# Kernel optimization log

Measured on AMD Instinct MI355X. Metric: run time of the kernel, lower is better.

The kernel has to match this reference:

```python
import jax, jax.numpy as jnp
import numpy as np

NEG_BIG = -1.0e9


def setup_inputs() -> dict:
    key = jax.random.key(0)
    kq, kk, kv, km = jax.random.split(key, 4)
    B, Lq, Lk, D = 16, 2048, 2048, 128
    queries = jax.random.normal(kq, (B, Lq, D), dtype=jnp.float32)
    keys = jax.random.normal(kk, (B, Lk, D), dtype=jnp.float32)
    values = jax.random.normal(kv, (B, Lk, D), dtype=jnp.float32)
    mask = (jax.random.uniform(km, (Lk,)) > 0.8).astype(jnp.float32)
    return {"queries": queries, "keys": keys, "values": values, "mask": mask}


def reference(queries, keys, values, mask):
    d = keys.shape[-1]
    # scores: [B, Lq, Lk]
    scores = jnp.einsum("bqd,bkd->bqk", queries, keys) / jnp.sqrt(jnp.float32(d))
    masked = scores + mask[None, None, :] * NEG_BIG
    attn = jax.nn.softmax(masked, axis=-1)
    # dropout is identity in eval / p=0.0
    return jnp.einsum("bqk,bkd->bqd", attn, values)
```

## Files before the change

### kernel.cpp

```cpp
#include <hip/hip_runtime.h>
#include <hip/hip_bf16.h>


#define B_    16
#define LQ_   2048
#define LK_   2048
#define DIM_  128
#define NTH   256
#define SCALE_ 0.08838834764831845f
#define LOG2E_ 1.4426950408889634f
#define SC2_   (SCALE_ * LOG2E_)
#define NEGBIG -1.0e9f
#define PS 72

typedef __attribute__((ext_vector_type(8))) short bf16x8;
typedef __attribute__((ext_vector_type(4))) float f32x4;

#define GLDS(gsrc, ldst) \
  __builtin_amdgcn_global_load_lds( \
      (const __attribute__((address_space(1))) unsigned int*)(gsrc), \
      (__attribute__((address_space(3))) unsigned int*)(ldst), 16, 0, 0)

#define MFMA16(A, Bv, C) __builtin_amdgcn_mfma_f32_16x16x32_bf16((A), (Bv), (C), 0, 0, 0)

static __device__ __forceinline__ unsigned short f2bf(float f) {
    unsigned int u = __builtin_bit_cast(unsigned int, f);
    u += 0x7fff + ((u >> 16) & 1);
    return (unsigned short)(u >> 16);
}

__global__ __launch_bounds__(256) void build_idx(const float* __restrict__ Mk,
                                                 int* __restrict__ hdr,
                                                 int* __restrict__ idx)
{
    __shared__ int sc[256];
    int t = threadIdx.x;
    int keep[8], loc[8];
    int c = 0;
    #pragma unroll
    for (int j = 0; j < 8; ++j) {
        keep[j] = (Mk[t * 8 + j] < 0.5f) ? 1 : 0;
        loc[j] = c;
        c += keep[j];
    }
    sc[t] = c;
    __syncthreads();
    for (int off = 1; off < 256; off <<= 1) {
        int v = (t >= off) ? sc[t - off] : 0;
        __syncthreads();
        sc[t] += v;
        __syncthreads();
    }
    int base = sc[t] - c;
    #pragma unroll
    for (int j = 0; j < 8; ++j)
        if (keep[j]) idx[base + loc[j]] = t * 8 + j;
    if (t == 255) hdr[0] = sc[255];
}

__global__ __launch_bounds__(NTH) void pack_kv(
    const float* __restrict__ K, const float* __restrict__ V,
    const int* __restrict__ hdr, const int* __restrict__ idx,
    unsigned short* __restrict__ Kb, unsigned short* __restrict__ Vtb)
{
    const int cnt = hdr[0];
    int bid = blockIdx.x;
    if (bid < 2048) {
        int gid = bid * NTH + threadIdx.x;
        int c  = gid & 15;
        int r2 = (gid >> 4) & 63;
        int T  = gid >> 10;
        int slot = (r2 & 32) + 2 * (r2 & 15) + ((r2 >> 4) & 1);
        int j = (T & 31) * 64 + slot;
        int key = (j < cnt) ? idx[j] : 0;
        const float4* s4 = (const float4*)(K + ((size_t)(T >> 5) * LK_ + key) * DIM_ + c * 8);
        float4 a = s4[0], bq = s4[1];
        bf16x8 h = { (short)f2bf(a.x),  (short)f2bf(a.y),  (short)f2bf(a.z),  (short)f2bf(a.w),
                     (short)f2bf(bq.x), (short)f2bf(bq.y), (short)f2bf(bq.z), (short)f2bf(bq.w) };
        *(bf16x8*)(Kb + (size_t)T * 8192 + r2 * 128 + ((c ^ (r2 & 15)) * 8)) = h;
    } else {
        int T = bid - 2048;
        int w4 = threadIdx.x >> 6, lane = threadIdx.x & 63;
        const float* vb = V + (size_t)(T >> 5) * LK_ * DIM_;
        const int* ix = idx + (T & 31) * 64;
        int jbase = (T & 31) * 64;
        unsigned short* db = Vtb + (size_t)T * 8192;
        #pragma unroll
        for (int half = 0; half < 2; ++half) {
            int d = half * 64 + lane;
            #pragma unroll
            for (int cb = 0; cb < 8; cb += 4) {
                int c = cb + w4;
                float v[8];
                #pragma unroll
                for (int kk = 0; kk < 8; ++kk) {
                    int j = c * 8 + kk;
                    int key = (jbase + j < cnt) ? ix[j] : 0;
                    v[kk] = vb[(size_t)key * DIM_ + d];
                }
                bf16x8 h = { (short)f2bf(v[0]), (short)f2bf(v[1]), (short)f2bf(v[2]), (short)f2bf(v[3]),
                             (short)f2bf(v[4]), (short)f2bf(v[5]), (short)f2bf(v[6]), (short)f2bf(v[7]) };
                *(bf16x8*)(db + (c >> 2) * 4096 + d * 32 + (c & 3) * 8) = h;
            }
        }
    }
}

__global__ __launch_bounds__(NTH, 2) void attn_mfma6(
    const float* __restrict__ Q, const unsigned short* __restrict__ Kb,
    const unsigned short* __restrict__ Vtb, const int* __restrict__ hdr,
    float* __restrict__ O)
{
    __shared__ __align__(16) unsigned short sKa[8192];
    __shared__ __align__(16) unsigned short sKb_[8192];
    __shared__ __align__(16) unsigned short sP[64 * PS];
    __shared__ float sLp[64];

    const int tid  = threadIdx.x;
    const int w    = tid >> 6, lane = tid & 63;
    const int quad = lane >> 4, l15 = lane & 15;
    const int rg   = (w & 1) * 32;
    const int wh   = w >> 1;
    const int kh   = wh * 32;

    const int bid = blockIdx.x;
    const int grp = bid >> 3;
    const int b   = (bid & 7) + 8 * (grp & 1);
    const int q0  = (grp >> 1) * 64;

    const int cnt = hdr[0];
    const int n = (((cnt + 63) >> 6) + 1) & ~1;

    bf16x8 vone;
    #pragma unroll
    for (int j = 0; j < 8; ++j) vone[j] = (short)0x3F80;

    const int voff = wh * 4096 + l15 * 32 + quad * 8;
    const unsigned short* vtb = Vtb + (size_t)(b * 32) * 8192 + voff;

    const char* kbase = (const char*)Kb + (size_t)(b * 32) * 16384;

    #pragma unroll
    for (int j = 0; j < 4; ++j) {
        int o = (j * 4 + w) * 1024;
        GLDS(kbase + o + lane * 16, (char*)sKa + o);
    }

    bf16x8 aQ[2][4];
    {
        const float4* Qg = (const float4*)(Q + ((size_t)b * LQ_ + q0) * DIM_);
        #pragma unroll
        for (int h = 0; h < 2; ++h) {
            #pragma unroll
            for (int it = 0; it < 4; ++it) {
                int i2 = tid + it * NTH;
                int r = i2 >> 5, c4 = i2 & 31;
                float4 v = Qg[(h * 32 + r) * 32 + c4];
                ushort4 hh = { f2bf(v.x * SC2_), f2bf(v.y * SC2_),
                               f2bf(v.z * SC2_), f2bf(v.w * SC2_) };
                *(ushort4*)&sP[r * 128 + (((c4 >> 1) ^ (r & 15)) * 8) + (c4 & 1) * 4] = hh;
            }
            __syncthreads();
            if ((rg >> 5) == h) {
                #pragma unroll
                for (int rs = 0; rs < 2; ++rs)
                    #pragma unroll
                    for (int ks = 0; ks < 4; ++ks)
                        aQ[rs][ks] = *(const bf16x8*)&sP[(rs * 16 + l15) * 128 +
                                                         (((ks * 4 + quad) ^ l15) * 8)];
            }
            __syncthreads();
        }
    }

    f32x4 acc[2][8], lacc[2];
    #pragma unroll
    for (int rs = 0; rs < 2; ++rs) {
        lacc[rs] = (f32x4){0.f, 0.f, 0.f, 0.f};
        #pragma unroll
        for (int dt = 0; dt < 8; ++dt) acc[rs][dt] = (f32x4){0.f, 0.f, 0.f, 0.f};
    }

    f32x4 s_[2][2];
    bf16x8 bvA[8], bvB[8];

#define QK_TILE(RD) do {                                                       \
    f32x4 c00 = (f32x4){0.f,0.f,0.f,0.f};                                      \
    f32x4 c01 = (f32x4){0.f,0.f,0.f,0.f};                                      \
    f32x4 c10 = (f32x4){0.f,0.f,0.f,0.f};                                      \
    f32x4 c11 = (f32x4){0.f,0.f,0.f,0.f};                                      \
    _Pragma("unroll")                                                          \
    for (int ks = 0; ks < 4; ++ks) {                                           \
        int co = ((ks * 4 + quad) ^ l15) * 8;                                  \
        bf16x8 bk0 = *(const bf16x8*)&(RD)[(kh + l15) * 128 + co];             \
        bf16x8 bk1 = *(const bf16x8*)&(RD)[(kh + 16 + l15) * 128 + co];        \
        c00 = MFMA16(aQ[0][ks], bk0, c00);                                     \
        c10 = MFMA16(aQ[1][ks], bk0, c10);                                     \
        c01 = MFMA16(aQ[0][ks], bk1, c01);                                     \
        c11 = MFMA16(aQ[1][ks], bk1, c11);                                     \
    }                                                                          \
    s_[0][0] = c00; s_[0][1] = c01; s_[1][0] = c10; s_[1][1] = c11;            \
} while (0)

#define SOFTMAX_AP(TI) do {                                                    \
    int slot0 = (TI) * 64 + kh + 2 * l15;                                      \
    unsigned umask = (slot0     < cnt ? 0x0000FFFFu : 0u) |                    \
                     (slot0 + 1 < cnt ? 0xFFFF0000u : 0u);                     \
    _Pragma("unroll")                                                          \
    for (int rs = 0; rs < 2; ++rs)                                             \
        _Pragma("unroll")                                                      \
        for (int r = 0; r < 4; ++r) {                                          \
            float p0 = __builtin_amdgcn_exp2f(s_[rs][0][r]);                   \
            float p1 = __builtin_amdgcn_exp2f(s_[rs][1][r]);                   \
            int row = rg + rs * 16 + quad * 4 + r;                             \
            unsigned pk = __builtin_amdgcn_perm(                               \
                __builtin_bit_cast(unsigned, p1),                              \
                __builtin_bit_cast(unsigned, p0), 0x07060302u) & umask;        \
            *(unsigned*)&sP[row * PS + kh + 2 * l15] = pk;                     \
        }                                                                      \
    aP0 = *(const bf16x8*)&sP[(rg + l15) * PS + kh + quad * 8];                \
    aP1 = *(const bf16x8*)&sP[(rg + 16 + l15) * PS + kh + quad * 8];           \
} while (0)

#define BODY(RD, WR, I, BVC, BVN) do {                                         \
    __syncthreads();                 \
    {                                                                          \
        const unsigned short* vsrc = vtb + (size_t)((I) + 1) * 8192;           \
        _Pragma("unroll")                                                      \
        for (int dt = 0; dt < 8; ++dt) BVN[dt] = *(const bf16x8*)(vsrc + dt * 512); \
    }                                                                          \
    {                                                                          \
        int t2 = (I) + 2; if (t2 > n - 1) t2 = n - 1;                          \
        const char* ksrc = kbase + (size_t)t2 * 16384;                         \
        _Pragma("unroll")                                                      \
        for (int j = 0; j < 4; ++j) {                                          \
            int o = (j * 4 + w) * 1024;                                        \
            GLDS(ksrc + o + lane * 16, (char*)(WR) + o);                       \
        }                                                                      \
    }                                                                          \
    bf16x8 aP0, aP1;                                                           \
    SOFTMAX_AP(I);                                                             \
    __builtin_amdgcn_s_setprio(1);                                             \
    QK_TILE(RD);                                      \
    lacc[0] = MFMA16(aP0, vone, lacc[0]);                                      \
    lacc[1] = MFMA16(aP1, vone, lacc[1]);                                      \
    _Pragma("unroll")                                                          \
    for (int dt = 0; dt < 8; ++dt) {                                           \
        acc[0][dt] = MFMA16(aP0, BVC[dt], acc[0][dt]);                         \
        acc[1][dt] = MFMA16(aP1, BVC[dt], acc[1][dt]);                         \
    }                                                                          \
    __builtin_amdgcn_s_setprio(0);                                             \
} while (0)

    {
        #pragma unroll
        for (int dt = 0; dt < 8; ++dt) bvA[dt] = *(const bf16x8*)(vtb + dt * 512);
        const char* ksrc = kbase + 16384;
        #pragma unroll
        for (int j = 0; j < 4; ++j) {
            int o = (j * 4 + w) * 1024;
            GLDS(ksrc + o + lane * 16, (char*)sKb_ + o);
        }
    }
    QK_TILE(sKa);

    int i = 0;
    for (; i + 1 < n - 1; i += 2) {
        BODY(sKb_, sKa, i,     bvA, bvB);
        BODY(sKa, sKb_, i + 1, bvB, bvA);
    }
    if (i < n - 1) BODY(sKb_, sKa, i, bvA, bvB);

    {
        bf16x8 aP0, aP1;
        SOFTMAX_AP(n - 1);
        lacc[0] = MFMA16(aP0, vone, lacc[0]);
        lacc[1] = MFMA16(aP1, vone, lacc[1]);
        #pragma unroll
        for (int dt = 0; dt < 8; ++dt) {
            acc[0][dt] = MFMA16(aP0, bvB[dt], acc[0][dt]);
            acc[1][dt] = MFMA16(aP1, bvB[dt], acc[1][dt]);
        }
    }
#undef BODY
#undef SOFTMAX_AP
#undef QK_TILE

    __syncthreads();

    float* sOw = (rg == 0) ? (float*)sKa : (float*)sKb_;
    if (wh == 1) {
        #pragma unroll
        for (int rs = 0; rs < 2; ++rs)
            #pragma unroll
            for (int r = 0; r < 4; ++r) {
                int lrow = rs * 16 + quad * 4 + r;
                #pragma unroll
                for (int dt = 0; dt < 8; ++dt)
                    sOw[lrow * 128 + dt * 16 + l15] = acc[rs][dt][r];
                if (l15 == 0) sLp[rg + lrow] = lacc[rs][r];
            }
    }
    __syncthreads();
    if (wh == 0) {
        float* Og = O + ((size_t)b * LQ_ + q0 + rg) * DIM_;
        #pragma unroll
        for (int rs = 0; rs < 2; ++rs)
            #pragma unroll
            for (int r = 0; r < 4; ++r) {
                int lrow = rs * 16 + quad * 4 + r;
                float inv = 1.0f / (lacc[rs][r] + sLp[rg + lrow]);
                #pragma unroll
                for (int dt = 0; dt < 8; ++dt)
                    Og[(size_t)lrow * DIM_ + dt * 16 + l15] =
                        (acc[rs][dt][r] + sOw[lrow * 128 + dt * 16 + l15]) * inv;
            }
    }
}

#define QS 136
#define VS 72
__global__ __launch_bounds__(NTH, 2) void attn_fallback(
    const float* __restrict__ Q, const float* __restrict__ K,
    const float* __restrict__ V, const float* __restrict__ Mk,
    float* __restrict__ O)
{
    __shared__ __align__(16) unsigned short sQ[64][QS];
    __shared__ __align__(16) unsigned short sK[64][QS];
    __shared__ __align__(16) unsigned short sVt[DIM_][VS];
    __shared__ __align__(16) unsigned short sPf[64][VS];
    __shared__ float sB[64];

    const int tid  = threadIdx.x;
    const int w    = tid >> 6, lane = tid & 63;
    const int quad = lane >> 4, l15 = lane & 15;
    const int bid = blockIdx.x;
    const int grp = bid >> 3;
    const int b   = (bid & 7) + 8 * (grp & 1);
    const int q0  = (grp >> 1) * 64;

    {
        const float4* Qg = (const float4*)(Q + ((size_t)b * LQ_ + q0) * DIM_);
        #pragma unroll
        for (int it = 0; it < 8; ++it) {
            int i = tid + it * NTH;
            int r = i >> 5, c4 = i & 31;
            float4 v = Qg[r * 32 + c4];
            ushort4 h = { f2bf(v.x), f2bf(v.y), f2bf(v.z), f2bf(v.w) };
            *(ushort4*)&sQ[r][c4 * 4] = h;
        }
    }
    __syncthreads();
    bf16x8 aQ[4];
    #pragma unroll
    for (int ks = 0; ks < 4; ++ks)
        aQ[ks] = *(const bf16x8*)&sQ[w * 16 + l15][ks * 32 + quad * 8];

    float m_i[4], l_i[4];
    f32x4 acc[8];
    #pragma unroll
    for (int r = 0; r < 4; ++r) { m_i[r] = -3.0e38f; l_i[r] = 0.f; }
    #pragma unroll
    for (int dt = 0; dt < 8; ++dt) acc[dt] = (f32x4){0.f, 0.f, 0.f, 0.f};

    for (int k0 = 0; k0 < LK_; k0 += 64) {
        const float4* Kg = (const float4*)(K + ((size_t)b * LK_ + k0) * DIM_);
        const float4* Vg = (const float4*)(V + ((size_t)b * LK_ + k0) * DIM_);
        #pragma unroll
        for (int it = 0; it < 8; ++it) {
            int i = tid + it * NTH;
            int r = i >> 5, c4 = i & 31;
            float4 kv = Kg[r * 32 + c4];
            ushort4 h = { f2bf(kv.x), f2bf(kv.y), f2bf(kv.z), f2bf(kv.w) };
            *(ushort4*)&sK[r][c4 * 4] = h;
            float4 vv = Vg[r * 32 + c4];
            int d = c4 * 4;
            sVt[d + 0][r] = f2bf(vv.x);
            sVt[d + 1][r] = f2bf(vv.y);
            sVt[d + 2][r] = f2bf(vv.z);
            sVt[d + 3][r] = f2bf(vv.w);
        }
        if (tid < 64) sB[tid] = Mk[k0 + tid] * NEGBIG;
        __syncthreads();

        f32x4 s[4];
        #pragma unroll
        for (int kt = 0; kt < 4; ++kt) {
            f32x4 c = (f32x4){0.f, 0.f, 0.f, 0.f};
            #pragma unroll
            for (int ks = 0; ks < 4; ++ks) {
                bf16x8 bk = *(const bf16x8*)&sK[kt * 16 + l15][ks * 32 + quad * 8];
                c = __builtin_amdgcn_mfma_f32_16x16x32_bf16(aQ[ks], bk, c, 0, 0, 0);
            }
            float bias = sB[kt * 16 + l15];
            #pragma unroll
            for (int r = 0; r < 4; ++r) s[kt][r] = c[r] * SCALE_ + bias;
        }
        #pragma unroll
        for (int r = 0; r < 4; ++r) {
            float mx = fmaxf(fmaxf(s[0][r], s[1][r]), fmaxf(s[2][r], s[3][r]));
            #pragma unroll
            for (int off = 1; off < 16; off <<= 1) mx = fmaxf(mx, __shfl_xor(mx, off));
            float mn = fmaxf(m_i[r], mx);
            float al = __expf(m_i[r] - mn);
            m_i[r] = mn;
            float rsum = 0.f;
            #pragma unroll
            for (int kt = 0; kt < 4; ++kt) {
                float p = __expf(s[kt][r] - mn);
                rsum += p;
                sPf[w * 16 + quad * 4 + r][kt * 16 + l15] = f2bf(p);
            }
            #pragma unroll
            for (int off = 1; off < 16; off <<= 1) rsum += __shfl_xor(rsum, off);
            l_i[r] = l_i[r] * al + rsum;
            #pragma unroll
            for (int dt = 0; dt < 8; ++dt) acc[dt][r] *= al;
        }
        bf16x8 aP0 = *(const bf16x8*)&sPf[w * 16 + l15][quad * 8];
        bf16x8 aP1 = *(const bf16x8*)&sPf[w * 16 + l15][32 + quad * 8];
        #pragma unroll
        for (int dt = 0; dt < 8; ++dt) {
            bf16x8 bv0 = *(const bf16x8*)&sVt[dt * 16 + l15][quad * 8];
            bf16x8 bv1 = *(const bf16x8*)&sVt[dt * 16 + l15][32 + quad * 8];
            acc[dt] = __builtin_amdgcn_mfma_f32_16x16x32_bf16(aP0, bv0, acc[dt], 0, 0, 0);
            acc[dt] = __builtin_amdgcn_mfma_f32_16x16x32_bf16(aP1, bv1, acc[dt], 0, 0, 0);
        }
        __syncthreads();
    }
    float* Og = O + ((size_t)b * LQ_ + q0 + w * 16) * DIM_;
    #pragma unroll
    for (int r = 0; r < 4; ++r) {
        float inv = 1.0f / l_i[r];
        int row = quad * 4 + r;
        #pragma unroll
        for (int dt = 0; dt < 8; ++dt)
            Og[(size_t)row * DIM_ + dt * 16 + l15] = acc[dt][r] * inv;
    }
}

extern "C" void kernel_launch(void* const* d_in, const int* in_sizes, int n_in,
                              void* d_out, int out_size, void* d_ws, size_t ws_size,
                              hipStream_t stream)
{
    const float* Q  = (const float*)d_in[0];
    const float* K  = (const float*)d_in[1];
    const float* V  = (const float*)d_in[2];
    const float* Mk = (const float*)d_in[3];
    float* O = (float*)d_out;

    const size_t seg  = (size_t)B_ * LK_ * DIM_ * 2;
    const size_t need = 16384 + 2 * seg;
    if (ws_size >= need) {
        int* hdr = (int*)d_ws;
        int* idx = hdr + 16;
        unsigned short* Kb  = (unsigned short*)((char*)d_ws + 16384);
        unsigned short* Vtb = Kb + seg / 2;
        hipLaunchKernelGGL(build_idx, dim3(1),    dim3(256), 0, stream, Mk, hdr, idx);
        hipLaunchKernelGGL(pack_kv,   dim3(2560), dim3(NTH), 0, stream, K, V, hdr, idx, Kb, Vtb);
        hipLaunchKernelGGL(attn_mfma6, dim3(512), dim3(NTH), 0, stream, Q, Kb, Vtb, hdr, O);
    } else {
        hipLaunchKernelGGL(attn_fallback, dim3(512), dim3(NTH), 0, stream, Q, K, V, Mk, O);
    }
}
```

Baseline: 146.9 us.

## Split attention block across eight waves with 16-row tiles and direct V loads

The attention kernel now runs 512 threads (eight waves) per block, and each wave owns 16 query rows instead of 32. This halves the per-wave accumulator and Q-fragment registers, and launch bounds ask for four blocks per CU to raise occupancy. The register double-buffered V prefetch is dropped: V fragments for the current tile are loaded inside each iteration, which may expose global-load latency. K tiles are loaded with fewer LDS copies per wave, while the per-tile MFMA count per wave halves and the QK B-operand LDS reads are duplicated across more waves.

```diff
diff --git a/kernel.cpp b/kernel.cpp
--- a/kernel.cpp
+++ b/kernel.cpp
@@ -7,6 +7,7 @@
 #define LK_   2048
 #define DIM_  128
 #define NTH   256
+#define ATH   512
 #define SCALE_ 0.08838834764831845f
 #define LOG2E_ 1.4426950408889634f
 #define SC2_   (SCALE_ * LOG2E_)
@@ -106,7 +107,7 @@
     }
 }
 
-__global__ __launch_bounds__(NTH, 2) void attn_mfma6(
+__global__ __launch_bounds__(ATH, 4) void attn_mfma8(
     const float* __restrict__ Q, const unsigned short* __restrict__ Kb,
     const unsigned short* __restrict__ Vtb, const int* __restrict__ hdr,
     float* __restrict__ O)
@@ -119,8 +120,8 @@
     const int tid  = threadIdx.x;
     const int w    = tid >> 6, lane = tid & 63;
     const int quad = lane >> 4, l15 = lane & 15;
-    const int rg   = (w & 1) * 32;
-    const int wh   = w >> 1;
+    const int rg   = (w & 3) * 16;
+    const int wh   = w >> 2;
     const int kh   = wh * 32;
 
     const int bid = blockIdx.x;
@@ -141,19 +142,19 @@
     const char* kbase = (const char*)Kb + (size_t)(b * 32) * 16384;
 
     #pragma unroll
-    for (int j = 0; j < 4; ++j) {
-        int o = (j * 4 + w) * 1024;
+    for (int j = 0; j < 2; ++j) {
+        int o = (j * 8 + w) * 1024;
         GLDS(kbase + o + lane * 16, (char*)sKa + o);
     }
 
-    bf16x8 aQ[2][4];
+    bf16x8 aQ[4];
     {
         const float4* Qg = (const float4*)(Q + ((size_t)b * LQ_ + q0) * DIM_);
         #pragma unroll
         for (int h = 0; h < 2; ++h) {
             #pragma unroll
-            for (int it = 0; it < 4; ++it) {
-                int i2 = tid + it * NTH;
+            for (int it = 0; it < 2; ++it) {
+                int i2 = tid + it * ATH;
                 int r = i2 >> 5, c4 = i2 & 31;
                 float4 v = Qg[(h * 32 + r) * 32 + c4];
                 ushort4 hh = { f2bf(v.x * SC2_), f2bf(v.y * SC2_),
@@ -163,43 +164,33 @@
             __syncthreads();
             if ((rg >> 5) == h) {
                 #pragma unroll
-                for (int rs = 0; rs < 2; ++rs)
-                    #pragma unroll
-                    for (int ks = 0; ks < 4; ++ks)
-                        aQ[rs][ks] = *(const bf16x8*)&sP[(rs * 16 + l15) * 128 +
-                                                         (((ks * 4 + quad) ^ l15) * 8)];
+                for (int ks = 0; ks < 4; ++ks)
+                    aQ[ks] = *(const bf16x8*)&sP[((rg & 16) + l15) * 128 +
+                                                 (((ks * 4 + quad) ^ l15) * 8)];
             }
             __syncthreads();
         }
     }
 
-    f32x4 acc[2][8], lacc[2];
-    #pragma unroll
-    for (int rs = 0; rs < 2; ++rs) {
-        lacc[rs] = (f32x4){0.f, 0.f, 0.f, 0.f};
-        #pragma unroll
-        for (int dt = 0; dt < 8; ++dt) acc[rs][dt] = (f32x4){0.f, 0.f, 0.f, 0.f};
-    }
-
-    f32x4 s_[2][2];
-    bf16x8 bvA[8], bvB[8];
+    f32x4 acc[8], lacc;
+    lacc = (f32x4){0.f, 0.f, 0.f, 0.f};
+    #pragma unroll
+    for (int dt = 0; dt < 8; ++dt) acc[dt] = (f32x4){0.f, 0.f, 0.f, 0.f};
+
+    f32x4 s_[2];
 
 #define QK_TILE(RD) do {                                                       \
-    f32x4 c00 = (f32x4){0.f,0.f,0.f,0.f};                                      \
-    f32x4 c01 = (f32x4){0.f,0.f,0.f,0.f};                                      \
-    f32x4 c10 = (f32x4){0.f,0.f,0.f,0.f};                                      \
-    f32x4 c11 = (f32x4){0.f,0.f,0.f,0.f};                                      \
+    f32x4 c0 = (f32x4){0.f,0.f,0.f,0.f};                                       \
+    f32x4 c1 = (f32x4){0.f,0.f,0.f,0.f};                                       \
     _Pragma("unroll")                                                          \
     for (int ks = 0; ks < 4; ++ks) {                                           \
         int co = ((ks * 4 + quad) ^ l15) * 8;                                  \
         bf16x8 bk0 = *(const bf16x8*)&(RD)[(kh + l15) * 128 + co];             \
         bf16x8 bk1 = *(const bf16x8*)&(RD)[(kh + 16 + l15) * 128 + co];        \
-        c00 = MFMA16(aQ[0][ks], bk0, c00);                                     \
-        c10 = MFMA16(aQ[1][ks], bk0, c10);                                     \
-        c01 = MFMA16(aQ[0][ks], bk1, c01);                                     \
-        c11 = MFMA16(aQ[1][ks], bk1, c11);                                     \
+        c0 = MFMA16(aQ[ks], bk0, c0);                                          \
+        c1 = MFMA16(aQ[ks], bk1, c1);                                          \
     }                                                                          \
-    s_[0][0] = c00; s_[0][1] = c01; s_[1][0] = c10; s_[1][1] = c11;            \
+    s_[0] = c0; s_[1] = c1;                                                    \
 } while (0)
 
 #define SOFTMAX_AP(TI) do {                                                    \
@@ -207,58 +198,49 @@
     unsigned umask = (slot0     < cnt ? 0x0000FFFFu : 0u) |                    \
                      (slot0 + 1 < cnt ? 0xFFFF0000u : 0u);                     \
     _Pragma("unroll")                                                          \
-    for (int rs = 0; rs < 2; ++rs)                                             \
-        _Pragma("unroll")                                                      \
-        for (int r = 0; r < 4; ++r) {                                          \
-            float p0 = __builtin_amdgcn_exp2f(s_[rs][0][r]);                   \
-            float p1 = __builtin_amdgcn_exp2f(s_[rs][1][r]);                   \
-            int row = rg + rs * 16 + quad * 4 + r;                             \
-            unsigned pk = __builtin_amdgcn_perm(                               \
-                __builtin_bit_cast(unsigned, p1),                              \
-                __builtin_bit_cast(unsigned, p0), 0x07060302u) & umask;        \
-            *(unsigned*)&sP[row * PS + kh + 2 * l15] = pk;                     \
-        }                                                                      \
-    aP0 = *(const bf16x8*)&sP[(rg + l15) * PS + kh + quad * 8];                \
-    aP1 = *(const bf16x8*)&sP[(rg + 16 + l15) * PS + kh + quad * 8];           \
+    for (int r = 0; r < 4; ++r) {                                              \
+        float p0 = __builtin_amdgcn_exp2f(s_[0][r]);                           \
+        float p1 = __builtin_amdgcn_exp2f(s_[1][r]);                           \
+        int row = rg + quad * 4 + r;                                           \
+        unsigned pk = __builtin_amdgcn_perm(                                   \
+            __builtin_bit_cast(unsigned, p1),                                  \
+            __builtin_bit_cast(unsigned, p0), 0x07060302u) & umask;            \
+        *(unsigned*)&sP[row * PS + kh + 2 * l15] = pk;                         \
+    }                                                                          \
+    aP = *(const bf16x8*)&sP[(rg + l15) * PS + kh + quad * 8];                 \
 } while (0)
 
-#define BODY(RD, WR, I, BVC, BVN) do {                                         \
-    __syncthreads();                 \
-    {                                                                          \
-        const unsigned short* vsrc = vtb + (size_t)((I) + 1) * 8192;           \
-        _Pragma("unroll")                                                      \
-        for (int dt = 0; dt < 8; ++dt) BVN[dt] = *(const bf16x8*)(vsrc + dt * 512); \
-    }                                                                          \
+#define BODY(RD, WR, I) do {                                                   \
+    __syncthreads();            \
+    const unsigned short* vsrc = vtb + (size_t)(I) * 8192;                     \
+    bf16x8 bv[8];                                                              \
+    _Pragma("unroll")                                                          \
+    for (int dt = 0; dt < 8; ++dt) bv[dt] = *(const bf16x8*)(vsrc + dt * 512); \
     {                                                                          \
         int t2 = (I) + 2; if (t2 > n - 1) t2 = n - 1;                          \
         const char* ksrc = kbase + (size_t)t2 * 16384;                         \
         _Pragma("unroll")                                                      \
-        for (int j = 0; j < 4; ++j) {                                          \
-            int o = (j * 4 + w) * 1024;                                        \
+        for (int j = 0; j < 2; ++j) {                                          \
+            int o = (j * 8 + w) * 1024;                                        \
             GLDS(ksrc + o + lane * 16, (char*)(WR) + o);                       \
         }                                                                      \
     }                                                                          \
-    bf16x8 aP0, aP1;                                                           \
+    bf16x8 aP;                                                                 \
     SOFTMAX_AP(I);                                                             \
     __builtin_amdgcn_s_setprio(1);                                             \
     QK_TILE(RD);                                      \
-    lacc[0] = MFMA16(aP0, vone, lacc[0]);                                      \
-    lacc[1] = MFMA16(aP1, vone, lacc[1]);                                      \
+    lacc = MFMA16(aP, vone, lacc);                                             \
     _Pragma("unroll")                                                          \
-    for (int dt = 0; dt < 8; ++dt) {                                           \
-        acc[0][dt] = MFMA16(aP0, BVC[dt], acc[0][dt]);                         \
-        acc[1][dt] = MFMA16(aP1, BVC[dt], acc[1][dt]);                         \
-    }                                                                          \
+    for (int dt = 0; dt < 8; ++dt)                                             \
+        acc[dt] = MFMA16(aP, bv[dt], acc[dt]);                                 \
     __builtin_amdgcn_s_setprio(0);                                             \
 } while (0)
 
     {
-        #pragma unroll
-        for (int dt = 0; dt < 8; ++dt) bvA[dt] = *(const bf16x8*)(vtb + dt * 512);
         const char* ksrc = kbase + 16384;
         #pragma unroll
-        for (int j = 0; j < 4; ++j) {
-            int o = (j * 4 + w) * 1024;
+        for (int j = 0; j < 2; ++j) {
+            int o = (j * 8 + w) * 1024;
             GLDS(ksrc + o + lane * 16, (char*)sKb_ + o);
         }
     }
@@ -266,21 +248,22 @@
 
     int i = 0;
     for (; i + 1 < n - 1; i += 2) {
-        BODY(sKb_, sKa, i,     bvA, bvB);
-        BODY(sKa, sKb_, i + 1, bvB, bvA);
-    }
-    if (i < n - 1) BODY(sKb_, sKa, i, bvA, bvB);
+        BODY(sKb_, sKa, i);
+        BODY(sKa, sKb_, i + 1);
+    }
+    if (i < n - 1) BODY(sKb_, sKa, i);
 
     {
-        bf16x8 aP0, aP1;
+        const unsigned short* vsrc = vtb + (size_t)(n - 1) * 8192;
+        bf16x8 bv[8];
+        #pragma unroll
+        for (int dt = 0; dt < 8; ++dt) bv[dt] = *(const bf16x8*)(vsrc + dt * 512);
+        bf16x8 aP;
         SOFTMAX_AP(n - 1);
-        lacc[0] = MFMA16(aP0, vone, lacc[0]);
-        lacc[1] = MFMA16(aP1, vone, lacc[1]);
-        #pragma unroll
-        for (int dt = 0; dt < 8; ++dt) {
-            acc[0][dt] = MFMA16(aP0, bvB[dt], acc[0][dt]);
-            acc[1][dt] = MFMA16(aP1, bvB[dt], acc[1][dt]);
-        }
+        lacc = MFMA16(aP, vone, lacc);
+        #pragma unroll
+        for (int dt = 0; dt < 8; ++dt)
+            acc[dt] = MFMA16(aP, bv[dt], acc[dt]);
     }
 #undef BODY
 #undef SOFTMAX_AP
@@ -288,33 +271,30 @@
 
     __syncthreads();
 
-    float* sOw = (rg == 0) ? (float*)sKa : (float*)sKb_;
+    float* sOw = (rg < 32) ? ((float*)sKa + (rg & 16) * 128)
+                           : ((float*)sKb_ + (rg & 16) * 128);
     if (wh == 1) {
         #pragma unroll
-        for (int rs = 0; rs < 2; ++rs)
-            #pragma unroll
-            for (int r = 0; r < 4; ++r) {
-                int lrow = rs * 16 + quad * 4 + r;
-                #pragma unroll
-                for (int dt = 0; dt < 8; ++dt)
-                    sOw[lrow * 128 + dt * 16 + l15] = acc[rs][dt][r];
-                if (l15 == 0) sLp[rg + lrow] = lacc[rs][r];
-            }
+        for (int r = 0; r < 4; ++r) {
+            int lrow = quad * 4 + r;
+            #pragma unroll
+            for (int dt = 0; dt < 8; ++dt)
+                sOw[lrow * 128 + dt * 16 + l15] = acc[dt][r];
+            if (l15 == 0) sLp[rg + lrow] = lacc[r];
+        }
     }
     __syncthreads();
     if (wh == 0) {
         float* Og = O + ((size_t)b * LQ_ + q0 + rg) * DIM_;
         #pragma unroll
-        for (int rs = 0; rs < 2; ++rs)
-            #pragma unroll
-            for (int r = 0; r < 4; ++r) {
-                int lrow = rs * 16 + quad * 4 + r;
-                float inv = 1.0f / (lacc[rs][r] + sLp[rg + lrow]);
-                #pragma unroll
-                for (int dt = 0; dt < 8; ++dt)
-                    Og[(size_t)lrow * DIM_ + dt * 16 + l15] =
-                        (acc[rs][dt][r] + sOw[lrow * 128 + dt * 16 + l15]) * inv;
-            }
+        for (int r = 0; r < 4; ++r) {
+            int lrow = quad * 4 + r;
+            float inv = 1.0f / (lacc[r] + sLp[rg + lrow]);
+            #pragma unroll
+            for (int dt = 0; dt < 8; ++dt)
+                Og[(size_t)lrow * DIM_ + dt * 16 + l15] =
+                    (acc[dt][r] + sOw[lrow * 128 + dt * 16 + l15]) * inv;
+        }
     }
 }
 
@@ -458,7 +438,7 @@
         unsigned short* Vtb = Kb + seg / 2;
         hipLaunchKernelGGL(build_idx, dim3(1),    dim3(256), 0, stream, Mk, hdr, idx);
         hipLaunchKernelGGL(pack_kv,   dim3(2560), dim3(NTH), 0, stream, K, V, hdr, idx, Kb, Vtb);
-        hipLaunchKernelGGL(attn_mfma6, dim3(512), dim3(NTH), 0, stream, Q, Kb, Vtb, hdr, O);
+        hipLaunchKernelGGL(attn_mfma8, dim3(512), dim3(ATH), 0, stream, Q, Kb, Vtb, hdr, O);
     } else {
         hipLaunchKernelGGL(attn_fallback, dim3(512), dim3(NTH), 0, stream, Q, K, V, Mk, O);
     }
```

Result: slower. 174.6 us (+18.9%).

## Load K tiles directly into registers in MFMA fragment layout, drop LDS staging

Applied to the files above, without the earlier changes.

The pack kernel now writes K in a per-lane MFMA-fragment order, so the attention kernel can load each lane's K operands straight from global memory into registers instead of staging them through LDS with global_load_lds. The K prefetch is double-buffered in registers (bkA/bkB), V loads move to the current iteration, and the software pipeline is restructured so QK runs before softmax each iteration, with the odd-tile epilogue simplified. This removes LDS traffic and the related bank-conflict and sync pressure for K, at the cost of more VGPRs and of exposing global load latency inside each iteration.

```diff
diff --git a/kernel.cpp b/kernel.cpp
--- a/kernel.cpp
+++ b/kernel.cpp
@@ -16,11 +16,6 @@
 typedef __attribute__((ext_vector_type(8))) short bf16x8;
 typedef __attribute__((ext_vector_type(4))) float f32x4;
 
-#define GLDS(gsrc, ldst) \
-  __builtin_amdgcn_global_load_lds( \
-      (const __attribute__((address_space(1))) unsigned int*)(gsrc), \
-      (__attribute__((address_space(3))) unsigned int*)(ldst), 16, 0, 0)
-
 #define MFMA16(A, Bv, C) __builtin_amdgcn_mfma_f32_16x16x32_bf16((A), (Bv), (C), 0, 0, 0)
 
 static __device__ __forceinline__ unsigned short f2bf(float f) {
@@ -68,16 +63,19 @@
     if (bid < 2048) {
         int gid = bid * NTH + threadIdx.x;
         int c  = gid & 15;
-        int r2 = (gid >> 4) & 63;
+        int s  = (gid >> 4) & 63;
         int T  = gid >> 10;
-        int slot = (r2 & 32) + 2 * (r2 & 15) + ((r2 >> 4) & 1);
-        int j = (T & 31) * 64 + slot;
+        int j = (T & 31) * 64 + s;
         int key = (j < cnt) ? idx[j] : 0;
         const float4* s4 = (const float4*)(K + ((size_t)(T >> 5) * LK_ + key) * DIM_ + c * 8);
         float4 a = s4[0], bq = s4[1];
         bf16x8 h = { (short)f2bf(a.x),  (short)f2bf(a.y),  (short)f2bf(a.z),  (short)f2bf(a.w),
                      (short)f2bf(bq.x), (short)f2bf(bq.y), (short)f2bf(bq.z), (short)f2bf(bq.w) };
-        *(bf16x8*)(Kb + (size_t)T * 8192 + r2 * 128 + ((c ^ (r2 & 15)) * 8)) = h;
+        int kc = s >> 5, kt2 = s & 1, l15v = (s >> 1) & 15;
+        int ks = c >> 2, quad = c & 3;
+        int lane = quad * 16 + l15v;
+        *(bf16x8*)(Kb + (size_t)T * 8192 +
+                   (size_t)(((kc * 2 + kt2) * 4 + ks) * 512 + lane * 8)) = h;
     } else {
         int T = bid - 2048;
         int w4 = threadIdx.x >> 6, lane = threadIdx.x & 63;
@@ -106,7 +104,7 @@
     }
 }
 
-__global__ __launch_bounds__(NTH, 2) void attn_mfma6(
+__global__ __launch_bounds__(NTH, 2) void attn_mfma10(
     const float* __restrict__ Q, const unsigned short* __restrict__ Kb,
     const unsigned short* __restrict__ Vtb, const int* __restrict__ hdr,
     float* __restrict__ O)
@@ -129,7 +127,7 @@
     const int q0  = (grp >> 1) * 64;
 
     const int cnt = hdr[0];
-    const int n = (((cnt + 63) >> 6) + 1) & ~1;
+    const int nt = (cnt + 63) >> 6;
 
     bf16x8 vone;
     #pragma unroll
@@ -137,14 +135,8 @@
 
     const int voff = wh * 4096 + l15 * 32 + quad * 8;
     const unsigned short* vtb = Vtb + (size_t)(b * 32) * 8192 + voff;
-
-    const char* kbase = (const char*)Kb + (size_t)(b * 32) * 16384;
-
-    #pragma unroll
-    for (int j = 0; j < 4; ++j) {
-        int o = (j * 4 + w) * 1024;
-        GLDS(kbase + o + lane * 16, (char*)sKa + o);
-    }
+    const int koff = wh * 4096 + lane * 8;
+    const unsigned short* ktb = Kb + (size_t)(b * 32) * 8192 + koff;
 
     bf16x8 aQ[2][4];
     {
@@ -181,23 +173,25 @@
         for (int dt = 0; dt < 8; ++dt) acc[rs][dt] = (f32x4){0.f, 0.f, 0.f, 0.f};
     }
 
-    f32x4 s_[2][2];
-    bf16x8 bvA[8], bvB[8];
-
-#define QK_TILE(RD) do {                                                       \
+    bf16x8 bkA[8], bkB[8];
+
+#define LOADK(BK, TI) do {                                                     \
+    const unsigned short* ksrc = ktb + (size_t)(TI) * 8192;                    \
+    _Pragma("unroll")                                                          \
+    for (int f = 0; f < 8; ++f) BK[f] = *(const bf16x8*)(ksrc + f * 512);      \
+} while (0)
+
+#define QK_TILE(BK) do {                                                       \
     f32x4 c00 = (f32x4){0.f,0.f,0.f,0.f};                                      \
     f32x4 c01 = (f32x4){0.f,0.f,0.f,0.f};                                      \
     f32x4 c10 = (f32x4){0.f,0.f,0.f,0.f};                                      \
     f32x4 c11 = (f32x4){0.f,0.f,0.f,0.f};                                      \
     _Pragma("unroll")                                                          \
     for (int ks = 0; ks < 4; ++ks) {                                           \
-        int co = ((ks * 4 + quad) ^ l15) * 8;                                  \
-        bf16x8 bk0 = *(const bf16x8*)&(RD)[(kh + l15) * 128 + co];             \
-        bf16x8 bk1 = *(const bf16x8*)&(RD)[(kh + 16 + l15) * 128 + co];        \
-        c00 = MFMA16(aQ[0][ks], bk0, c00);                                     \
-        c10 = MFMA16(aQ[1][ks], bk0, c10);                                     \
-        c01 = MFMA16(aQ[0][ks], bk1, c01);                                     \
-        c11 = MFMA16(aQ[1][ks], bk1, c11);                                     \
+        c00 = MFMA16(aQ[0][ks], BK[ks], c00);                                  \
+        c10 = MFMA16(aQ[1][ks], BK[ks], c10);                                  \
+        c01 = MFMA16(aQ[0][ks], BK[4 + ks], c01);                              \
+        c11 = MFMA16(aQ[1][ks], BK[4 + ks], c11);                              \
     }                                                                          \
     s_[0][0] = c00; s_[0][1] = c01; s_[1][0] = c10; s_[1][1] = c11;            \
 } while (0)
@@ -222,71 +216,40 @@
     aP1 = *(const bf16x8*)&sP[(rg + 16 + l15) * PS + kh + quad * 8];           \
 } while (0)
 
-#define BODY(RD, WR, I, BVC, BVN) do {                                         \
-    __syncthreads();                 \
-    {                                                                          \
-        const unsigned short* vsrc = vtb + (size_t)((I) + 1) * 8192;           \
-        _Pragma("unroll")                                                      \
-        for (int dt = 0; dt < 8; ++dt) BVN[dt] = *(const bf16x8*)(vsrc + dt * 512); \
-    }                                                                          \
-    {                                                                          \
-        int t2 = (I) + 2; if (t2 > n - 1) t2 = n - 1;                          \
-        const char* ksrc = kbase + (size_t)t2 * 16384;                         \
-        _Pragma("unroll")                                                      \
-        for (int j = 0; j < 4; ++j) {                                          \
-            int o = (j * 4 + w) * 1024;                                        \
-            GLDS(ksrc + o + lane * 16, (char*)(WR) + o);                       \
-        }                                                                      \
-    }                                                                          \
+#define BODY(CUR, NXT, I) do {                                                 \
+    const unsigned short* vsrc = vtb + (size_t)(I) * 8192;                     \
+    bf16x8 bv[8];                                                              \
+    _Pragma("unroll")                                                          \
+    for (int dt = 0; dt < 8; ++dt) bv[dt] = *(const bf16x8*)(vsrc + dt * 512); \
+    int t2 = (I) + 1; if (t2 > nt - 1) t2 = nt - 1;                            \
+    LOADK(NXT, t2);                                                            \
+    f32x4 s_[2][2];                                                            \
     bf16x8 aP0, aP1;                                                           \
+    QK_TILE(CUR);                                                              \
     SOFTMAX_AP(I);                                                             \
     __builtin_amdgcn_s_setprio(1);                                             \
-    QK_TILE(RD);                                      \
     lacc[0] = MFMA16(aP0, vone, lacc[0]);                                      \
     lacc[1] = MFMA16(aP1, vone, lacc[1]);                                      \
     _Pragma("unroll")                                                          \
     for (int dt = 0; dt < 8; ++dt) {                                           \
-        acc[0][dt] = MFMA16(aP0, BVC[dt], acc[0][dt]);                         \
-        acc[1][dt] = MFMA16(aP1, BVC[dt], acc[1][dt]);                         \
+        acc[0][dt] = MFMA16(aP0, bv[dt], acc[0][dt]);                          \
+        acc[1][dt] = MFMA16(aP1, bv[dt], acc[1][dt]);                          \
     }                                                                          \
     __builtin_amdgcn_s_setprio(0);                                             \
+    __syncthreads();                                                           \
 } while (0)
 
-    {
-        #pragma unroll
-        for (int dt = 0; dt < 8; ++dt) bvA[dt] = *(const bf16x8*)(vtb + dt * 512);
-        const char* ksrc = kbase + 16384;
-        #pragma unroll
-        for (int j = 0; j < 4; ++j) {
-            int o = (j * 4 + w) * 1024;
-            GLDS(ksrc + o + lane * 16, (char*)sKb_ + o);
-        }
-    }
-    QK_TILE(sKa);
-
+    LOADK(bkA, 0);
     int i = 0;
-    for (; i + 1 < n - 1; i += 2) {
-        BODY(sKb_, sKa, i,     bvA, bvB);
-        BODY(sKa, sKb_, i + 1, bvB, bvA);
-    }
-    if (i < n - 1) BODY(sKb_, sKa, i, bvA, bvB);
-
-    {
-        bf16x8 aP0, aP1;
-        SOFTMAX_AP(n - 1);
-        lacc[0] = MFMA16(aP0, vone, lacc[0]);
-        lacc[1] = MFMA16(aP1, vone, lacc[1]);
-        #pragma unroll
-        for (int dt = 0; dt < 8; ++dt) {
-            acc[0][dt] = MFMA16(aP0, bvB[dt], acc[0][dt]);
-            acc[1][dt] = MFMA16(aP1, bvB[dt], acc[1][dt]);
-        }
-    }
+    for (; i + 2 <= nt; i += 2) {
+        BODY(bkA, bkB, i);
+        BODY(bkB, bkA, i + 1);
+    }
+    if (i < nt) BODY(bkA, bkB, i);
 #undef BODY
 #undef SOFTMAX_AP
 #undef QK_TILE
-
-    __syncthreads();
+#undef LOADK
 
     float* sOw = (rg == 0) ? (float*)sKa : (float*)sKb_;
     if (wh == 1) {
@@ -458,7 +421,7 @@
         unsigned short* Vtb = Kb + seg / 2;
         hipLaunchKernelGGL(build_idx, dim3(1),    dim3(256), 0, stream, Mk, hdr, idx);
         hipLaunchKernelGGL(pack_kv,   dim3(2560), dim3(NTH), 0, stream, K, V, hdr, idx, Kb, Vtb);
-        hipLaunchKernelGGL(attn_mfma6, dim3(512), dim3(NTH), 0, stream, Q, Kb, Vtb, hdr, O);
+        hipLaunchKernelGGL(attn_mfma10, dim3(512), dim3(NTH), 0, stream, Q, Kb, Vtb, hdr, O);
     } else {
         hipLaunchKernelGGL(attn_fallback, dim3(512), dim3(NTH), 0, stream, Q, K, V, Mk, O);
     }
```

Result: no change. 149.5 us (+1.8%).
